# Kernel optimization log

Measured on AMD Instinct MI355X. Metric: run time of the kernel, lower is better.

Reference implementation:

```python
import jax, jax.numpy as jnp
import numpy as np

N, L, D, H = 2, 2048, 1024, 16
DK = D // H  # 64


def setup_inputs() -> dict:
    key = jax.random.key(0)
    ks = jax.random.split(key, 8)
    Xq = jax.random.normal(ks[0], (N, L, D), dtype=jnp.float32)
    Xk = jax.random.normal(ks[1], (N, L, D), dtype=jnp.float32)
    Xv = jax.random.normal(ks[2], (N, L, D), dtype=jnp.float32)
    mask_2d = jax.random.randint(ks[3], (N, L, L), 0, 2, dtype=jnp.int32)
    scale = 0.02
    Wq = jax.random.normal(ks[4], (D, D), dtype=jnp.float32) * scale
    Wk = jax.random.normal(ks[5], (D, D), dtype=jnp.float32) * scale
    Wv = jax.random.normal(ks[6], (D, D), dtype=jnp.float32) * scale
    Wo = jax.random.normal(ks[7], (D, D), dtype=jnp.float32) * scale
    return {"Xq": Xq, "Xk": Xk, "Xv": Xv, "Wq": Wq, "Wk": Wk, "Wv": Wv, "Wo": Wo, "mask_2d": mask_2d}


def reference(Xq, Xk, Xv, Wq, Wk, Wv, Wo, mask_2d):
    # Projections (bias=False). Per-head slicing in the original == reshape to [N,L,H,DK].
    Q = (Xq @ Wq).reshape(N, L, H, DK)
    K = (Xk @ Wk).reshape(N, L, H, DK)
    V = (Xv @ Wv).reshape(N, L, H, DK)
    # Scaled dot-product scores: [N, H, L, L]
    scores = jnp.einsum("blhd,bmhd->bhlm", Q, K) / jnp.sqrt(jnp.asarray(DK, scores_dtype(Q)))
    # NOTE: original uses masked_fill(mask==0, 0) BEFORE softmax (zero-fill, not -inf).
    scores = jnp.where(mask_2d[:, None, :, :] == 0, jnp.zeros((), scores.dtype), scores)
    A = jax.nn.softmax(scores, axis=-1)
    O = jnp.einsum("bhlm,bmhd->blhd", A, V).reshape(N, L, D)
    return O @ Wo


def scores_dtype(Q):
    return Q.dtype
```

## Files before the change

kernel.cpp:

```cpp
#include <hip/hip_runtime.h>
#include <hip/hip_bf16.h>

#define NB 2
#define L_SEQ 2048
#define NH 16
#define DKH 64
#define DMODEL 1024
#define MROWS (NB * L_SEQ)
#define QSCALE 0.18033688f
#define DD (DMODEL * DMODEL)

typedef __attribute__((ext_vector_type(8))) short short8;
typedef __attribute__((ext_vector_type(4))) float f32x4;

static __device__ __forceinline__ unsigned short f2bf(float f) {
    unsigned u = __float_as_uint(f);
    u += 0x7fffu + ((u >> 16) & 1u);
    return (unsigned short)(u >> 16);
}

static __device__ __forceinline__ float fexp2(float x) {
#if __has_builtin(__builtin_amdgcn_exp2f)
    return __builtin_amdgcn_exp2f(x);
#else
    return __expf(x * 0.6931471806f);
#endif
}

static __device__ __forceinline__ unsigned pk_bf16(float a, float b) {
    __hip_bfloat162 h = __float22bfloat162_rn(make_float2(a, b));
    return *reinterpret_cast<unsigned*>(&h);
}

static __device__ __forceinline__ void gll16(const void* g, void* l) {
    __builtin_amdgcn_global_load_lds(
        (const __attribute__((address_space(1))) void*)g,
        (__attribute__((address_space(3))) void*)l, 16, 0, 0);
}

__global__ __launch_bounds__(256)
void prep(const float* __restrict__ Xq, const float* __restrict__ Xk,
          const float* __restrict__ Xv, const float* __restrict__ w0,
          const float* __restrict__ w1, const float* __restrict__ w2,
          const float* __restrict__ w3, const int* __restrict__ mask,
          unsigned short* __restrict__ XB, unsigned short* __restrict__ WtB,
          unsigned long long* __restrict__ MWT)
{
    __shared__ float ts[32][33];
    const int bx = blockIdx.x;
    const int t  = threadIdx.x;

    if (bx < 12288) {
        const int z = bx >> 12;
        const float* src = (z == 0) ? Xq : (z == 1) ? Xk : Xv;
        const size_t i4 = (size_t)(bx & 4095) * 256 + t;
        float4 v = ((const float4*)src)[i4];
        ushort4 o;
        o.x = f2bf(v.x); o.y = f2bf(v.y); o.z = f2bf(v.z); o.w = f2bf(v.w);
        ((ushort4*)(XB + (size_t)z * 4194304))[i4] = o;
    } else if (bx < 16384) {
        const int idx = bx - 12288;
        const int z   = idx >> 10;
        const int rem = idx & 1023;
        const float* W = (z == 0) ? w0 : (z == 1) ? w1 : (z == 2) ? w2 : w3;
        unsigned short* Wt = WtB + (size_t)z * DD;
        const int n0 = (rem & 31) * 32;
        const int k0 = (rem >> 5) * 32;
        const int r  = t >> 3;
        const int c  = (t & 7) * 4;
        float4 v = *(const float4*)&W[(size_t)(k0 + r) * DMODEL + n0 + c];
        ts[r][c + 0] = v.x; ts[r][c + 1] = v.y;
        ts[r][c + 2] = v.z; ts[r][c + 3] = v.w;
        __syncthreads();
        ushort4 o;
        o.x = f2bf(ts[c + 0][r]); o.y = f2bf(ts[c + 1][r]);
        o.z = f2bf(ts[c + 2][r]); o.w = f2bf(ts[c + 3][r]);
        *(ushort4*)&Wt[(size_t)(n0 + r) * DMODEL + k0 + c] = o;
    } else {
        const int lane = t & 63;
        const size_t wid = (size_t)(bx - 16384) * 4 + (t >> 6);
        const int mv = mask[wid * 64 + lane];
        const unsigned long long bits = __ballot(mv != 0);
        if (lane == 0) {
            const int b   = (int)(wid >> 16);
            const int rem = (int)(wid & 65535);
            const int row = rem >> 5;
            const int wd  = rem & 31;
            MWT[((size_t)b * 32 + wd) * L_SEQ + row] = bits;
        }
    }
}

__global__ __launch_bounds__(256)
void gemm_qkv(const unsigned short* __restrict__ XB,
              const unsigned short* __restrict__ WtB,
              unsigned short* __restrict__ QKV)
{
    __shared__ __align__(16) unsigned short SMEM[16384];

    const int t    = threadIdx.x;
    const int w    = t >> 6;
    const int lane = t & 63;

    const int bid   = blockIdx.x;
    const int xcd   = bid & 7;
    const int idx   = bid >> 3;
    const int pair  = xcd * 12 + (idx >> 3);
    const int n0    = (idx & 7) * 128;
    const int m0    = (pair & 31) * 128;
    const int z     = pair >> 5;

    const unsigned short* A = XB  + (size_t)z * ((size_t)MROWS * DMODEL);
    const unsigned short* B = WtB + (size_t)z * DD;

    const int srow = lane >> 2;
    const int sc4  = (lane & 3) ^ (srow & 3);

    const unsigned short* ag[2];
    const unsigned short* bg[2];
    int lao[2], lbo[2];
#pragma unroll
    for (int g = 0; g < 2; ++g) {
        const int R = w * 32 + g * 16;
        ag[g] = A + (size_t)(m0 + R + srow) * DMODEL + sc4 * 8;
        bg[g] = B + (size_t)(n0 + R + srow) * DMODEL + sc4 * 8;
        lao[g] = R * 32;
        lbo[g] = R * 32;
    }

    const int ml = lane & 15;
    const int q  = lane >> 4;
    const int wm = (w >> 1) * 64;
    const int wn = (w & 1) * 64;

    const f32x4 z4 = {0.f, 0.f, 0.f, 0.f};
    f32x4 acc[4][4];
#pragma unroll
    for (int i = 0; i < 4; ++i)
#pragma unroll
        for (int j = 0; j < 4; ++j) acc[i][j] = z4;

#pragma unroll
    for (int g = 0; g < 2; ++g) {
        gll16(ag[g], &SMEM[lao[g]]);
        gll16(bg[g], &SMEM[8192 + lbo[g]]);
    }

    for (int j = 0; j < 32; ++j) {
        const int cur = j & 1;
        __syncthreads();
        if (j < 31) {
            const int kt = (j + 1) * 32;
            const int nb = (cur ^ 1) * 4096;
#pragma unroll
            for (int g = 0; g < 2; ++g) {
                gll16(ag[g] + kt, &SMEM[nb + lao[g]]);
                gll16(bg[g] + kt, &SMEM[8192 + nb + lbo[g]]);
            }
        }
        const unsigned short* As = &SMEM[cur * 4096];
        const unsigned short* Bs = &SMEM[8192 + cur * 4096];
        short8 av[4], bv[4];
#pragma unroll
        for (int mt = 0; mt < 4; ++mt)
            av[mt] = *(const short8*)
                &As[(wm + mt * 16 + ml) * 32 + ((q ^ (ml & 3)) * 8)];
#pragma unroll
        for (int nt = 0; nt < 4; ++nt)
            bv[nt] = *(const short8*)
                &Bs[(wn + nt * 16 + ml) * 32 + ((q ^ (ml & 3)) * 8)];
#pragma unroll
        for (int mt = 0; mt < 4; ++mt)
#pragma unroll
            for (int nt = 0; nt < 4; ++nt)
                acc[mt][nt] = __builtin_amdgcn_mfma_f32_16x16x32_bf16(
                    av[mt], bv[nt], acc[mt][nt], 0, 0, 0);
    }

    unsigned short* O = QKV + (size_t)z * ((size_t)MROWS * DMODEL);
    __syncthreads();
    unsigned short* Ts = SMEM;

    if (z == 2) {
#pragma unroll
        for (int mt = 0; mt < 4; ++mt) {
            const int trow0 = wm + mt * 16 + q * 4;
            const int ch    = trow0 >> 3;
#pragma unroll
            for (int nt = 0; nt < 4; ++nt) {
                const int tcol = wn + nt * 16 + ml;
                const int pc   = (ch & 8) | ((ch & 7) ^ (tcol & 7));
                ushort4 pv;
                pv.x = f2bf(acc[mt][nt][0]); pv.y = f2bf(acc[mt][nt][1]);
                pv.z = f2bf(acc[mt][nt][2]); pv.w = f2bf(acc[mt][nt][3]);
                *(ushort4*)&Ts[tcol * 128 + pc * 8 + (trow0 & 7)] = pv;
            }
        }
        __syncthreads();
        const int bb = m0 >> 11;
        const int l0 = (m0 & (L_SEQ - 1)) + (t & 15) * 8;
        const int cr = t & 15;
#pragma unroll
        for (int it = 0; it < 8; ++it) {
            const int tcol = (t >> 4) + 16 * it;
            const int pc   = (cr & 8) | ((cr & 7) ^ (tcol & 7));
            short8 vv = *(const short8*)&Ts[tcol * 128 + pc * 8];
            const int n  = n0 + tcol;
            const int hh = n >> 6;
            const int dk = n & (DKH - 1);
            *(short8*)&O[((size_t)(bb * NH + hh) * DKH + dk) * L_SEQ + l0] = vv;
        }
    } else {
        const float qs = (z == 0) ? QSCALE : 1.0f;
#pragma unroll
        for (int mt = 0; mt < 4; ++mt) {
            const int row0 = wm + mt * 16 + q * 4;
#pragma unroll
            for (int nt = 0; nt < 4; ++nt) {
                const int col = wn + nt * 16 + ml;
#pragma unroll
                for (int r = 0; r < 4; ++r)
                    Ts[(row0 + r) * 128 + col] = f2bf(acc[mt][nt][r] * qs);
            }
        }
        __syncthreads();
        const int mloc = t >> 3;
        const int c0   = t & 7;
#pragma unroll
        for (int pass = 0; pass < 4; ++pass) {
#pragma unroll
            for (int half = 0; half < 2; ++half) {
                const int m = mloc + 32 * pass;
                const int c = c0 + 8 * half;
                short8 v = *(const short8*)&Ts[m * 128 + c * 8];
                const int row = m0 + m;
                const int bb  = row >> 11;
                const int l   = row & (L_SEQ - 1);
                const int n   = n0 + c * 8;
                const int hh  = n >> 6;
                const int dk  = n & (DKH - 1);
                *(short8*)&O[(((size_t)(bb * NH + hh) * L_SEQ + l) << 6) + dk] = v;
            }
        }
    }
}

__global__ __launch_bounds__(256)
void gemm_out(const unsigned short* __restrict__ OB,
              const unsigned short* __restrict__ Wt,
              float* __restrict__ out)
{
    __shared__ __align__(16) unsigned short As[2][2048];
    __shared__ __align__(16) unsigned short Bs[2][4096];

    const int t    = threadIdx.x;
    const int w    = t >> 6;
    const int lane = t & 63;

    const int bid = blockIdx.x;
    const int xcd = bid & 7;
    const int idx = bid >> 3;
    const int n0  = (idx & 7) * 128;
    const int m0  = (xcd * 8 + (idx >> 3)) * 64;

    const int srow = lane >> 2;
    const int sc4  = (lane & 3) ^ (srow & 3);

    const unsigned short* ag =
        OB + (size_t)(m0 + w * 16 + srow) * DMODEL + sc4 * 8;
    const unsigned short* bg[2];
    int lbo[2];
#pragma unroll
    for (int g = 0; g < 2; ++g) {
        const int R = w * 32 + g * 16;
        bg[g] = Wt + (size_t)(n0 + R + srow) * DMODEL + sc4 * 8;
        lbo[g] = R * 32;
    }
    const int lao = (w * 16) * 32;

    const int ml = lane & 15;
    const int q  = lane >> 4;
    const int wm = (w >> 1) * 32;
    const int wn = (w & 1) * 64;

    const f32x4 z4 = {0.f, 0.f, 0.f, 0.f};
    f32x4 acc[2][4];
#pragma unroll
    for (int i = 0; i < 2; ++i)
#pragma unroll
        for (int j = 0; j < 4; ++j) acc[i][j] = z4;

    gll16(ag, &As[0][lao]);
#pragma unroll
    for (int g = 0; g < 2; ++g) gll16(bg[g], &Bs[0][lbo[g]]);

    for (int j = 0; j < 32; ++j) {
        const int cur = j & 1;
        __syncthreads();
        if (j < 31) {
            const int kt = (j + 1) * 32;
            gll16(ag + kt, &As[cur ^ 1][lao]);
#pragma unroll
            for (int g = 0; g < 2; ++g)
                gll16(bg[g] + kt, &Bs[cur ^ 1][lbo[g]]);
        }
        short8 av[2], bv[4];
#pragma unroll
        for (int mt = 0; mt < 2; ++mt)
            av[mt] = *(const short8*)
                &As[cur][(wm + mt * 16 + ml) * 32 + ((q ^ (ml & 3)) * 8)];
#pragma unroll
        for (int nt = 0; nt < 4; ++nt)
            bv[nt] = *(const short8*)
                &Bs[cur][(wn + nt * 16 + ml) * 32 + ((q ^ (ml & 3)) * 8)];
#pragma unroll
        for (int mt = 0; mt < 2; ++mt)
#pragma unroll
            for (int nt = 0; nt < 4; ++nt)
                acc[mt][nt] = __builtin_amdgcn_mfma_f32_16x16x32_bf16(
                    av[mt], bv[nt], acc[mt][nt], 0, 0, 0);
    }

#pragma unroll
    for (int mt = 0; mt < 2; ++mt) {
        const int gr0 = m0 + wm + mt * 16 + q * 4;
#pragma unroll
        for (int nt = 0; nt < 4; ++nt) {
            const int col = n0 + wn + nt * 16 + ml;
#pragma unroll
            for (int r = 0; r < 4; ++r)
                out[(size_t)(gr0 + r) * DMODEL + col] = acc[mt][nt][r];
        }
    }
}

__global__ __launch_bounds__(256, 4)
void attn_mfma(const unsigned short* __restrict__ Qb,
               const unsigned short* __restrict__ Kb,
               const unsigned short* __restrict__ Vtb,
               const unsigned long long* __restrict__ MWT,
               unsigned short* __restrict__ OB)
{
    __shared__ __align__(16) unsigned short Qs[64 * 64];
    __shared__ __align__(16) unsigned short Ks[64 * 64];
    __shared__ __align__(16) unsigned short Vts[64 * 64];
    __shared__ __align__(16) unsigned short Ps[4][16 * 64];
    __shared__ __align__(16) unsigned long long MskL[64];

    const int t    = threadIdx.x;
    const int w    = t >> 6;
    const int lane = t & 63;
    const int ml   = lane & 15;
    const int quad = lane >> 4;

    const int bid = blockIdx.x;
    const int p   = (bid >> 8) * 8 + (bid & 7);
    const int jq  = (bid >> 3) & 31;
    const int h   = p & 15;
    const int b   = p >> 4;
    const int q0  = jq * 64;

    const size_t hoff = (size_t)(b * NH + h) * L_SEQ * DKH;
    const unsigned short* Qh  = Qb  + hoff;
    const unsigned short* Kh  = Kb  + hoff;
    const unsigned short* Vth = Vtb + hoff;

    const int srow = lane >> 3;
    const int sc   = (lane & 7) ^ srow;

    gll16(Qh + (size_t)(q0 + w * 16 + srow) * DKH + sc * 8, &Qs[(w * 16) * 64]);
    gll16(Qh + (size_t)(q0 + w * 16 + 8 + srow) * DKH + sc * 8, &Qs[(w * 16 + 8) * 64]);
    __syncthreads();

    short8 qf[2];
#pragma unroll
    for (int s = 0; s < 2; ++s)
        qf[s] = *(const short8*)
            &Qs[(w * 16 + ml) * 64 + (((s * 4 + quad) ^ (ml & 7)) * 8)];

    const unsigned short* kg0 = Kh + (size_t)(w * 16 + srow) * DKH + sc * 8;
    const unsigned short* kg1 = Kh + (size_t)(w * 16 + 8 + srow) * DKH + sc * 8;
    const unsigned short* vg0 = Vth + (size_t)(w * 16 + srow) * L_SEQ + sc * 8;
    const unsigned short* vg1 = Vth + (size_t)(w * 16 + 8 + srow) * L_SEQ + sc * 8;
    unsigned short* lk0 = &Ks[(w * 16) * 64];
    unsigned short* lk1 = &Ks[(w * 16 + 8) * 64];
    unsigned short* lv0 = &Vts[(w * 16) * 64];
    unsigned short* lv1 = &Vts[(w * 16 + 8) * 64];

    const unsigned long long* mg = MWT + (size_t)b * 32 * L_SEQ + q0 + t;
    unsigned long long m_pf = 0;
    if (t < 64) m_pf = mg[0];

    f32x4 oacc[4];
    const f32x4 z4 = {0.f, 0.f, 0.f, 0.f};
#pragma unroll
    for (int dt = 0; dt < 4; ++dt) oacc[dt] = z4;
    float l_i = 0.f;

    for (int j = 0; j < 32; ++j) {
        __syncthreads();
        gll16(kg0, lk0);  gll16(kg1, lk1);
        gll16(vg0, lv0);  gll16(vg1, lv1);
        kg0 += 64 * DKH;  kg1 += 64 * DKH;
        vg0 += 64;        vg1 += 64;
        if (t < 64) {
            MskL[t] = m_pf;
            if (j < 31) m_pf = mg[(size_t)(j + 1) * L_SEQ];
        }
        __syncthreads();

        f32x4 sacc[4];
#pragma unroll
        for (int kt = 0; kt < 4; ++kt) sacc[kt] = z4;
#pragma unroll
        for (int s = 0; s < 2; ++s) {
            short8 kf[4];
#pragma unroll
            for (int kt = 0; kt < 4; ++kt)
                kf[kt] = *(const short8*)
                    &Ks[(kt * 16 + ml) * 64 + (((s * 4 + quad) ^ (ml & 7)) * 8)];
#pragma unroll
            for (int kt = 0; kt < 4; ++kt)
                sacc[kt] = __builtin_amdgcn_mfma_f32_16x16x32_bf16(
                    kf[kt], qf[s], sacc[kt], 0, 0, 0);
        }

        const unsigned long long wq = MskL[w * 16 + ml] >> (quad * 4);
        const unsigned mlo = (unsigned)wq;
        const unsigned mhi = (unsigned)(wq >> 32);
        float rs = 0.f;
        float pr[4][4];
#pragma unroll
        for (int kt = 0; kt < 4; ++kt) {
            const unsigned word = (kt < 2) ? mlo : mhi;
            const int base = (kt & 1) * 16;
#pragma unroll
            for (int r = 0; r < 4; ++r) {
                const float mf = (float)((word >> (base + r)) & 1u);
                const float e  = fexp2(sacc[kt][r] * mf);
                pr[kt][r] = e;
                rs += e;
            }
        }
        rs += __shfl_xor(rs, 16);
        rs += __shfl_xor(rs, 32);
        l_i += rs;
#pragma unroll
        for (int kt = 0; kt < 4; ++kt) {
            uint2 pk;
            pk.x = pk_bf16(pr[kt][0], pr[kt][1]);
            pk.y = pk_bf16(pr[kt][2], pr[kt][3]);
            const int cp = (kt * 2 + (quad >> 1)) ^ (ml & 7);
            *(uint2*)&Ps[w][ml * 64 + cp * 8 + (quad & 1) * 4] = pk;
        }

#pragma unroll
        for (int s = 0; s < 2; ++s) {
            const short8 pf = *(const short8*)
                &Ps[w][ml * 64 + (((s * 4 + quad) ^ (ml & 7)) * 8)];
#pragma unroll
            for (int dt = 0; dt < 4; ++dt) {
                const short8 vf = *(const short8*)
                    &Vts[(dt * 16 + ml) * 64 + (((s * 4 + quad) ^ (ml & 7)) * 8)];
                oacc[dt] = __builtin_amdgcn_mfma_f32_16x16x32_bf16(
                    vf, pf, oacc[dt], 0, 0, 0);
            }
        }
    }

    const float inv = 1.0f / l_i;
    const int qrow = q0 + w * 16 + ml;
#pragma unroll
    for (int dt = 0; dt < 4; ++dt) {
        ushort4 o4;
        o4.x = f2bf(oacc[dt][0] * inv);
        o4.y = f2bf(oacc[dt][1] * inv);
        o4.z = f2bf(oacc[dt][2] * inv);
        o4.w = f2bf(oacc[dt][3] * inv);
        *(ushort4*)&OB[(size_t)(b * L_SEQ + qrow) * DMODEL + h * DKH +
                       dt * 16 + quad * 4] = o4;
    }
}

extern "C" void kernel_launch(void* const* d_in, const int* in_sizes, int n_in,
                              void* d_out, int out_size, void* d_ws, size_t ws_size,
                              hipStream_t stream)
{
    (void)in_sizes; (void)n_in; (void)out_size; (void)ws_size;

    const float* Xq   = (const float*)d_in[0];
    const float* Xk   = (const float*)d_in[1];
    const float* Xv   = (const float*)d_in[2];
    const float* Wq   = (const float*)d_in[3];
    const float* Wk   = (const float*)d_in[4];
    const float* Wv   = (const float*)d_in[5];
    const float* Wo   = (const float*)d_in[6];
    const int*   mask = (const int*)d_in[7];
    float* out = (float*)d_out;

    char* base = (char*)d_ws;
    unsigned short*     XB  = (unsigned short*)base;
    unsigned short*     WtB = (unsigned short*)(base + (24u << 20));
    unsigned short*     QKV = (unsigned short*)(base + (32u << 20));
    unsigned short*     OB  = (unsigned short*)(base + (56u << 20));
    unsigned long long* MWT = (unsigned long long*)(base + (64u << 20));

    const size_t tsz = (size_t)MROWS * DMODEL;

    prep<<<dim3(49152), 256, 0, stream>>>(
        Xq, Xk, Xv, Wq, Wk, Wv, Wo, mask, XB, WtB, MWT);

    gemm_qkv<<<dim3(768), 256, 0, stream>>>(XB, WtB, QKV);

    attn_mfma<<<dim3(1024), 256, 0, stream>>>(
        QKV, QKV + tsz, QKV + 2 * tsz, MWT, OB);

    gemm_out<<<dim3(512), 256, 0, stream>>>(OB, WtB + 3 * (size_t)DD, out);
}
```

Baseline: 264.5 us.

## Register-prefetch K/V tiles in attention and coarsen mask-packing blocks in prep

The attention loop no longer uses direct global-to-LDS loads. It now loads the next K/V tile into registers right after the barrier, so the global load overlaps the MFMA compute, and writes those registers to LDS at the top of the next iteration. Separately, the mask bit-packing part of prep has each block process 8 wavefront-chunks, which shrinks the prep grid from 49152 to 20480 blocks. The change trades extra VGPRs and explicit LDS stores for latency hiding and fewer launched blocks.

```diff
diff --git a/kernel.cpp b/kernel.cpp
--- a/kernel.cpp
+++ b/kernel.cpp
@@ -78,15 +78,19 @@
         *(ushort4*)&Wt[(size_t)(n0 + r) * DMODEL + k0 + c] = o;
     } else {
         const int lane = t & 63;
-        const size_t wid = (size_t)(bx - 16384) * 4 + (t >> 6);
-        const int mv = mask[wid * 64 + lane];
-        const unsigned long long bits = __ballot(mv != 0);
-        if (lane == 0) {
-            const int b   = (int)(wid >> 16);
-            const int rem = (int)(wid & 65535);
-            const int row = rem >> 5;
-            const int wd  = rem & 31;
-            MWT[((size_t)b * 32 + wd) * L_SEQ + row] = bits;
+        const size_t wbase = (size_t)(bx - 16384) * 4 + (t >> 6);
+#pragma unroll
+        for (int it = 0; it < 8; ++it) {
+            const size_t wid = wbase + (size_t)it * 16384;
+            const int mv = mask[wid * 64 + lane];
+            const unsigned long long bits = __ballot(mv != 0);
+            if (lane == 0) {
+                const int b   = (int)(wid >> 16);
+                const int rem = (int)(wid & 65535);
+                const int row = rem >> 5;
+                const int wd  = rem & 31;
+                MWT[((size_t)b * 32 + wd) * L_SEQ + row] = bits;
+            }
         }
     }
 }
@@ -382,15 +386,20 @@
     const unsigned short* kg1 = Kh + (size_t)(w * 16 + 8 + srow) * DKH + sc * 8;
     const unsigned short* vg0 = Vth + (size_t)(w * 16 + srow) * L_SEQ + sc * 8;
     const unsigned short* vg1 = Vth + (size_t)(w * 16 + 8 + srow) * L_SEQ + sc * 8;
-    unsigned short* lk0 = &Ks[(w * 16) * 64];
-    unsigned short* lk1 = &Ks[(w * 16 + 8) * 64];
-    unsigned short* lv0 = &Vts[(w * 16) * 64];
-    unsigned short* lv1 = &Vts[(w * 16 + 8) * 64];
+    unsigned short* lk0 = &Ks[(w * 16) * 64 + lane * 8];
+    unsigned short* lk1 = &Ks[(w * 16 + 8) * 64 + lane * 8];
+    unsigned short* lv0 = &Vts[(w * 16) * 64 + lane * 8];
+    unsigned short* lv1 = &Vts[(w * 16 + 8) * 64 + lane * 8];
 
     const unsigned long long* mg = MWT + (size_t)b * 32 * L_SEQ + q0 + t;
     unsigned long long m_pf = 0;
     if (t < 64) m_pf = mg[0];
 
+    short8 kr0 = *(const short8*)kg0;  kg0 += 64 * DKH;
+    short8 kr1 = *(const short8*)kg1;  kg1 += 64 * DKH;
+    short8 vr0 = *(const short8*)vg0;  vg0 += 64;
+    short8 vr1 = *(const short8*)vg1;  vg1 += 64;
+
     f32x4 oacc[4];
     const f32x4 z4 = {0.f, 0.f, 0.f, 0.f};
 #pragma unroll
@@ -399,15 +408,19 @@
 
     for (int j = 0; j < 32; ++j) {
         __syncthreads();
-        gll16(kg0, lk0);  gll16(kg1, lk1);
-        gll16(vg0, lv0);  gll16(vg1, lv1);
-        kg0 += 64 * DKH;  kg1 += 64 * DKH;
-        vg0 += 64;        vg1 += 64;
-        if (t < 64) {
-            MskL[t] = m_pf;
-            if (j < 31) m_pf = mg[(size_t)(j + 1) * L_SEQ];
-        }
-        __syncthreads();
+        *(short8*)lk0 = kr0;
+        *(short8*)lk1 = kr1;
+        *(short8*)lv0 = vr0;
+        *(short8*)lv1 = vr1;
+        if (t < 64) MskL[t] = m_pf;
+        __syncthreads();
+        if (j < 31) {
+            kr0 = *(const short8*)kg0;  kg0 += 64 * DKH;
+            kr1 = *(const short8*)kg1;  kg1 += 64 * DKH;
+            vr0 = *(const short8*)vg0;  vg0 += 64;
+            vr1 = *(const short8*)vg1;  vg1 += 64;
+            if (t < 64) m_pf = mg[(size_t)(j + 1) * L_SEQ];
+        }
 
         f32x4 sacc[4];
 #pragma unroll
@@ -507,7 +520,7 @@
 
     const size_t tsz = (size_t)MROWS * DMODEL;
 
-    prep<<<dim3(49152), 256, 0, stream>>>(
+    prep<<<dim3(20480), 256, 0, stream>>>(
         Xq, Xk, Xv, Wq, Wk, Wv, Wo, mask, XB, WtB, MWT);
 
     gemm_qkv<<<dim3(768), 256, 0, stream>>>(XB, WtB, QKV);
```

New measurement: 256.6 us. 1.03x faster.
